# Kernel tuning notes

Measured on AMD Instinct MI355X. Metric: run time of the kernel, lower is better.

Reference implementation:

```python
import jax, jax.numpy as jnp
import numpy as np

FEATURE_SIZE = 1000000  # padding index == FEATURE_SIZE
NEG_INF = -1e9


def _attn_pool(emb_table, hist_idx, ad_idx):
    # hist_idx: [B, L] int, ad_idx: [B] int
    hist = emb_table[hist_idx]          # [B, L, K] gather
    ad = emb_table[ad_idx]              # [B, K]
    score = jnp.einsum('blk,bk->bl', hist, ad)          # [B, L]
    score = jnp.where(hist_idx != FEATURE_SIZE, score, NEG_INF)
    w = jax.nn.softmax(score, axis=1)
    return jnp.einsum('blk,bl->bk', hist, w)            # [B, K]


def setup_inputs() -> dict:
    key = jax.random.key(0)
    ks = jax.random.split(key, 12)
    B, F, K = 4096, 8, 64
    V = FEATURE_SIZE + 1
    d_in = 3 * K + F * K  # 704
    inp = {
        'feature_idx': jax.random.randint(ks[0], (B, F), 0, FEATURE_SIZE),
        'hist_item': jax.random.randint(ks[1], (B, 350), 0, V),
        'hist_author': jax.random.randint(ks[2], (B, 250), 0, V),
        'hist_music': jax.random.randint(ks[3], (B, 100), 0, V),
        'emb_table': jax.random.normal(ks[4], (V, K), jnp.float32),
        'W1': jax.random.normal(ks[5], (d_in, 512), jnp.float32) * 0.02,
        'b1': jnp.zeros((512,), jnp.float32),
        'W2': jax.random.normal(ks[6], (512, 256), jnp.float32) * 0.02,
        'b2': jnp.zeros((256,), jnp.float32),
        'W3': jax.random.normal(ks[7], (256, 128), jnp.float32) * 0.02,
        'b3': jnp.zeros((128,), jnp.float32),
        'Wo': jax.random.normal(ks[8], (128, 1), jnp.float32) * 0.02,
        'bo': jnp.zeros((1,), jnp.float32),
    }
    return inp


def reference(feature_idx, hist_item, hist_author, hist_music, emb_table,
              W1, b1, W2, b2, W3, b3, Wo, bo):
    # ad indices for the three behavior features: columns 2, 3, 6
    pools = [
        _attn_pool(emb_table, hist_item, feature_idx[:, 2]),
        _attn_pool(emb_table, hist_author, feature_idx[:, 3]),
        _attn_pool(emb_table, hist_music, feature_idx[:, 6]),
    ]
    user_beha = jnp.concatenate(pools, axis=1)                    # [B, 3K]
    B = feature_idx.shape[0]
    ad_emb = emb_table[feature_idx].reshape(B, -1)                # [B, F*K]
    x = jnp.concatenate([user_beha, ad_emb], axis=1)              # [B, 704]
    x = jax.nn.relu(x @ W1 + b1)
    x = jax.nn.relu(x @ W2 + b2)
    x = jax.nn.relu(x @ W3 + b3)
    logits = x @ Wo + bo                                          # [B, 1]
    return logits
```

## Files before the change

### kernel.cpp

```cpp
#include <hip/hip_runtime.h>
#include <cstddef>

#define BATCH   4096
#define PAD_IDX 1000000
#define NEG_INF_F (-1e9f)
#define EMB_FLOATS 64000064

typedef __attribute__((ext_vector_type(8))) short bf16x8;
typedef __attribute__((ext_vector_type(4))) float f32x4;
typedef unsigned short u16;

__device__ __forceinline__ u16 f2bf(float f) {
    unsigned u = __float_as_uint(f);
    return (u16)((u + 0x7fffu + ((u >> 16) & 1u)) >> 16);
}

#define UPD(mm, dd, aa, s, v)                          \
    {                                                  \
        float nm = fmaxf(mm, (s));                     \
        float sc = __expf(mm - nm);                    \
        float e  = __expf((s) - nm);                   \
        dd = fmaf(dd, sc, e);                          \
        aa.x = fmaf(aa.x, sc, e * (v).x);              \
        aa.y = fmaf(aa.y, sc, e * (v).y);              \
        aa.z = fmaf(aa.z, sc, e * (v).z);              \
        aa.w = fmaf(aa.w, sc, e * (v).w);              \
        mm = nm;                                       \
    }

#define MERGE(P)                                                  \
    {                                                             \
        float mo  = __shfl_xor(m, P);                             \
        float d_o = __shfl_xor(d, P);                             \
        float ax = __shfl_xor(acc.x, P);                          \
        float ay = __shfl_xor(acc.y, P);                          \
        float az = __shfl_xor(acc.z, P);                          \
        float aw = __shfl_xor(acc.w, P);                          \
        float nm = fmaxf(m, mo);                                  \
        float sA = __expf(m - nm), sB = __expf(mo - nm);          \
        d = d * sA + d_o * sB;                                    \
        acc.x = acc.x * sA + ax * sB;                             \
        acc.y = acc.y * sA + ay * sB;                             \
        acc.z = acc.z * sA + az * sB;                             \
        acc.w = acc.w * sA + aw * sB;                             \
        m = nm;                                                   \
    }

#define QRED(s)                       \
    s += __shfl_xor(s, 1);            \
    s += __shfl_xor(s, 2);            \
    s += __shfl_xor(s, 4);            \
    s += __shfl_xor(s, 8);

#define DOT4(v, a) ((v).x * (a).x + (v).y * (a).y + (v).z * (a).z + (v).w * (a).w)

__global__ void __launch_bounds__(256) prep_kernel(
    const int* __restrict__ fidx,
    const int* __restrict__ hist_item,
    const int* __restrict__ hist_author,
    const int* __restrict__ hist_music,
    const float* __restrict__ emb,
    const float* __restrict__ W1, const float* __restrict__ W2, const float* __restrict__ W3,
    u16* __restrict__ x,
    u16* __restrict__ w1t, u16* __restrict__ w2t, u16* __restrict__ w3t)
{
    __shared__ float tile[32][33];
    const int blk = blockIdx.x;
    const int tid = threadIdx.x;

    if (blk < 2048) {
        float s = 0.f;
        const size_t base = (size_t)blk * 32768 + tid * 4;
#pragma unroll 8
        for (int i = 0; i < 32; ++i) {
            const size_t fi = base + (size_t)i * 1024;
            if (fi + 4 <= EMB_FLOATS) {
                const float4 v = *(const float4*)(emb + fi);
                s += v.x + v.y + v.z + v.w;
            }
        }
        if (s == 1.2345e37f) x[0] = 1;
        return;
    }

    if (blk < 7168) {
        const int w    = (blk - 2048) * 4 + (tid >> 6);
        const int lane = tid & 63;
        const int t16  = lane & 15;
        const int q    = lane >> 4;

        if (w < 3 * BATCH) {
            const int h = w >> 12;
            const int b = w & (BATCH - 1);
            int L, col, off;
            const int* hrow;
            if (h == 0)      { L = 350; col = 2; off = 0;   hrow = hist_item   + (size_t)b * 350; }
            else if (h == 1) { L = 250; col = 3; off = 64;  hrow = hist_author + (size_t)b * 250; }
            else             { L = 100; col = 6; off = 128; hrow = hist_music  + (size_t)b * 100; }

            const int ad_idx = fidx[b * 8 + col];
            const float4 ad4 = *(const float4*)(emb + (size_t)ad_idx * 64 + 4 * t16);

            float m = NEG_INF_F, d = 0.f;
            float4 acc = make_float4(0.f, 0.f, 0.f, 0.f);
            float mB = NEG_INF_F, dB = 0.f;
            float4 aB = make_float4(0.f, 0.f, 0.f, 0.f);

            int l = 0;
            if (L >= 16) {
                int n0 = hrow[q], n1 = hrow[4 + q], n2 = hrow[8 + q], n3 = hrow[12 + q];
                while (true) {
                    const int i0 = n0, i1 = n1, i2 = n2, i3 = n3;
                    const float4 v0 = *(const float4*)(emb + (size_t)i0 * 64 + 4 * t16);
                    const float4 v1 = *(const float4*)(emb + (size_t)i1 * 64 + 4 * t16);
                    const float4 v2 = *(const float4*)(emb + (size_t)i2 * 64 + 4 * t16);
                    const float4 v3 = *(const float4*)(emb + (size_t)i3 * 64 + 4 * t16);
                    l += 16;
                    const bool more = (l + 16 <= L);
                    if (more) {
                        n0 = hrow[l + q];      n1 = hrow[l + 4 + q];
                        n2 = hrow[l + 8 + q];  n3 = hrow[l + 12 + q];
                    }
                    float s0 = DOT4(v0, ad4);
                    float s1 = DOT4(v1, ad4);
                    float s2 = DOT4(v2, ad4);
                    float s3 = DOT4(v3, ad4);
                    QRED(s0) QRED(s1) QRED(s2) QRED(s3)
                    if (i0 == PAD_IDX) s0 = NEG_INF_F;
                    if (i1 == PAD_IDX) s1 = NEG_INF_F;
                    if (i2 == PAD_IDX) s2 = NEG_INF_F;
                    if (i3 == PAD_IDX) s3 = NEG_INF_F;
                    UPD(m, d, acc, s0, v0)
                    UPD(mB, dB, aB, s1, v1)
                    UPD(m, d, acc, s2, v2)
                    UPD(mB, dB, aB, s3, v3)
                    if (!more) break;
                }
            }
            for (; l < L; l += 4) {
                const int li = l + q;
                const int i0 = (li < L) ? hrow[li] : PAD_IDX;
                const float4 v0 = *(const float4*)(emb + (size_t)i0 * 64 + 4 * t16);
                float s0 = DOT4(v0, ad4);
                QRED(s0)
                if (i0 == PAD_IDX) s0 = NEG_INF_F;
                UPD(m, d, acc, s0, v0)
            }

            {
                float nm = fmaxf(m, mB);
                float eA = __expf(m - nm), eB = __expf(mB - nm);
                d = d * eA + dB * eB;
                acc.x = acc.x * eA + aB.x * eB;
                acc.y = acc.y * eA + aB.y * eB;
                acc.z = acc.z * eA + aB.z * eB;
                acc.w = acc.w * eA + aB.w * eB;
                m = nm;
            }
            MERGE(16)
            MERGE(32)

            if (lane < 16) {
                const float inv = 1.f / d;
                uint2 p;
                p.x = (unsigned)f2bf(acc.x * inv) | ((unsigned)f2bf(acc.y * inv) << 16);
                p.y = (unsigned)f2bf(acc.z * inv) | ((unsigned)f2bf(acc.w * inv) << 16);
                *(uint2*)(x + (size_t)b * 704 + off + 4 * t16) = p;
            }
        } else {
            const int tt = w - 3 * BATCH;
            const int b  = tt >> 1;
            const int f  = ((tt & 1) << 2) + q;
            const int idx = fidx[b * 8 + f];
            const float4 v = *(const float4*)(emb + (size_t)idx * 64 + 4 * t16);
            uint2 p;
            p.x = (unsigned)f2bf(v.x) | ((unsigned)f2bf(v.y) << 16);
            p.y = (unsigned)f2bf(v.z) | ((unsigned)f2bf(v.w) << 16);
            *(uint2*)(x + (size_t)b * 704 + 192 + (size_t)f * 64 + 4 * t16) = p;
        }
        return;
    }

    int t = blk - 7168;
    const float* W; u16* WT; int K, N, tk, tn;
    if (t < 352)      { W = W1; WT = w1t; K = 704; N = 512; tk = t % 22; tn = t / 22; }
    else if (t < 480) { t -= 352; W = W2; WT = w2t; K = 512; N = 256; tk = t % 16; tn = t / 16; }
    else              { t -= 480; W = W3; WT = w3t; K = 256; N = 128; tk = t % 8;  tn = t / 8;  }
    const int k0 = tk * 32, n0 = tn * 32;
    const int tx = tid & 31, ty = tid >> 5;
#pragma unroll
    for (int j = 0; j < 4; ++j)
        tile[ty + 8 * j][tx] = W[(size_t)(k0 + ty + 8 * j) * N + n0 + tx];
    __syncthreads();
#pragma unroll
    for (int j = 0; j < 4; ++j)
        WT[(size_t)(n0 + ty + 8 * j) * K + k0 + tx] = f2bf(tile[tx][ty + 8 * j]);
}

template <int BN>
__global__ void __launch_bounds__(256) gemm_mfma(
    const u16* __restrict__ A, const u16* __restrict__ BT,
    const float* __restrict__ bias, u16* __restrict__ C,
    int M, int N, int K)
{
    constexpr int NB = BN / 16;
    __shared__ u16 As[64][40];
    __shared__ u16 Bs[BN][40];

    const int tid  = threadIdx.x;
    const int wave = tid >> 6, lane = tid & 63;
    const int quad = lane >> 4, l16 = lane & 15;
    const int bm = blockIdx.y * 64, bn = blockIdx.x * BN;

    const int srow = tid >> 2;
    const int sk   = (tid & 3) * 8;

    f32x4 acc[NB];
#pragma unroll
    for (int i = 0; i < NB; ++i) acc[i] = (f32x4){0.f, 0.f, 0.f, 0.f};

    const size_t a_base = (size_t)(bm + srow) * K + sk;

    for (int k0 = 0; k0 < K; k0 += 32) {
        *(float4*)&As[srow][sk] = *(const float4*)(A + a_base + k0);
#pragma unroll
        for (int r0 = 0; r0 < BN; r0 += 64) {
            *(float4*)&Bs[r0 + srow][sk] =
                *(const float4*)(BT + (size_t)(bn + r0 + srow) * K + k0 + sk);
        }
        __syncthreads();

        const bf16x8 af = *(const bf16x8*)&As[wave * 16 + l16][quad * 8];
#pragma unroll
        for (int ni = 0; ni < NB; ++ni) {
            const bf16x8 bf = *(const bf16x8*)&Bs[ni * 16 + l16][quad * 8];
            acc[ni] = __builtin_amdgcn_mfma_f32_16x16x32_bf16(af, bf, acc[ni], 0, 0, 0);
        }
        __syncthreads();
    }

#pragma unroll
    for (int ni = 0; ni < NB; ++ni) {
        const int col = bn + ni * 16 + l16;
        const float bv = bias[col];
#pragma unroll
        for (int r = 0; r < 4; ++r) {
            const int row = bm + wave * 16 + quad * 4 + r;
            float v = fmaxf(acc[ni][r] + bv, 0.f);
            C[(size_t)row * N + col] = f2bf(v);
        }
    }
}

__global__ void __launch_bounds__(256) tail_mlp(
    const u16* __restrict__ h1, const u16* __restrict__ W2T, const u16* __restrict__ W3T,
    const float* __restrict__ b2, const float* __restrict__ b3,
    const float* __restrict__ Wo, const float* __restrict__ bo,
    float* __restrict__ out)
{
    __shared__ u16 As16[16][40];
    __shared__ u16 Bs[256][40];
    __shared__ u16 h2s[16][264];
    __shared__ float psum[16][4];

    const int tid  = threadIdx.x;
    const int wave = tid >> 6, lane = tid & 63;
    const int quad = lane >> 4, l16 = lane & 15;
    const int r0 = blockIdx.x * 16;

    f32x4 acc2[4];
#pragma unroll
    for (int i = 0; i < 4; ++i) acc2[i] = (f32x4){0.f, 0.f, 0.f, 0.f};

    for (int k0 = 0; k0 < 512; k0 += 32) {
        if (tid < 64)
            *(float4*)&As16[tid >> 2][(tid & 3) * 8] =
                *(const float4*)(h1 + (size_t)(r0 + (tid >> 2)) * 512 + k0 + (tid & 3) * 8);
        {
            const u16* src = W2T + (size_t)tid * 512 + k0;
#pragma unroll
            for (int c = 0; c < 4; ++c)
                *(float4*)&Bs[tid][c * 8] = *(const float4*)(src + c * 8);
        }
        __syncthreads();

        const bf16x8 af = *(const bf16x8*)&As16[l16][quad * 8];
#pragma unroll
        for (int ni = 0; ni < 4; ++ni) {
            const bf16x8 bf = *(const bf16x8*)&Bs[wave * 64 + ni * 16 + l16][quad * 8];
            acc2[ni] = __builtin_amdgcn_mfma_f32_16x16x32_bf16(af, bf, acc2[ni], 0, 0, 0);
        }
        __syncthreads();
    }

#pragma unroll
    for (int ni = 0; ni < 4; ++ni) {
        const int col = wave * 64 + ni * 16 + l16;
        const float bv = b2[col];
#pragma unroll
        for (int r = 0; r < 4; ++r)
            h2s[quad * 4 + r][col] = f2bf(fmaxf(acc2[ni][r] + bv, 0.f));
    }
    __syncthreads();

    f32x4 acc3[2];
#pragma unroll
    for (int i = 0; i < 2; ++i) acc3[i] = (f32x4){0.f, 0.f, 0.f, 0.f};

    for (int k0 = 0; k0 < 256; k0 += 32) {
        if (tid < 128) {
            const u16* src = W3T + (size_t)tid * 256 + k0;
#pragma unroll
            for (int c = 0; c < 4; ++c)
                *(float4*)&Bs[tid][c * 8] = *(const float4*)(src + c * 8);
        }
        __syncthreads();

        const bf16x8 af = *(const bf16x8*)&h2s[l16][k0 + quad * 8];
#pragma unroll
        for (int ni = 0; ni < 2; ++ni) {
            const bf16x8 bf = *(const bf16x8*)&Bs[wave * 32 + ni * 16 + l16][quad * 8];
            acc3[ni] = __builtin_amdgcn_mfma_f32_16x16x32_bf16(af, bf, acc3[ni], 0, 0, 0);
        }
        __syncthreads();
    }

    float part[4] = {0.f, 0.f, 0.f, 0.f};
#pragma unroll
    for (int ni = 0; ni < 2; ++ni) {
        const int col = wave * 32 + ni * 16 + l16;
        const float bv = b3[col];
        const float wv = Wo[col];
#pragma unroll
        for (int r = 0; r < 4; ++r)
            part[r] = fmaf(fmaxf(acc3[ni][r] + bv, 0.f), wv, part[r]);
    }
#pragma unroll
    for (int r = 0; r < 4; ++r) { QRED(part[r]) }
    if (l16 == 0) {
#pragma unroll
        for (int r = 0; r < 4; ++r)
            psum[quad * 4 + r][wave] = part[r];
    }
    __syncthreads();
    if (tid < 16)
        out[r0 + tid] = psum[tid][0] + psum[tid][1] + psum[tid][2] + psum[tid][3] + bo[0];
}

extern "C" void kernel_launch(void* const* d_in, const int* in_sizes, int n_in,
                              void* d_out, int out_size, void* d_ws, size_t ws_size,
                              hipStream_t stream) {
    const int*   fidx  = (const int*)d_in[0];
    const int*   hitem = (const int*)d_in[1];
    const int*   hauth = (const int*)d_in[2];
    const int*   hmus  = (const int*)d_in[3];
    const float* emb   = (const float*)d_in[4];
    const float* W1 = (const float*)d_in[5];
    const float* b1 = (const float*)d_in[6];
    const float* W2 = (const float*)d_in[7];
    const float* b2 = (const float*)d_in[8];
    const float* W3 = (const float*)d_in[9];
    const float* b3 = (const float*)d_in[10];
    const float* Wo = (const float*)d_in[11];
    const float* bo = (const float*)d_in[12];
    float* out = (float*)d_out;

    u16* x   = (u16*)d_ws;
    u16* h1  = x   + (size_t)BATCH * 704;
    u16* w1t = h1  + (size_t)BATCH * 512;
    u16* w2t = w1t + (size_t)704 * 512;
    u16* w3t = w2t + (size_t)512 * 256;

    prep_kernel<<<7680, 256, 0, stream>>>(fidx, hitem, hauth, hmus, emb,
                                          W1, W2, W3, x, w1t, w2t, w3t);

    gemm_mfma<64><<<dim3(512 / 64, BATCH / 64), 256, 0, stream>>>(
        x, w1t, b1, h1, BATCH, 512, 704);

    tail_mlp<<<BATCH / 16, 256, 0, stream>>>(h1, w2t, w3t, b2, b3, Wo, bo, out);
}
```

Measured before the change: 503.8 us.

## Fuse first MLP layer into tail kernel and drop full embedding-table sweep

Removes the 2048 prep blocks that streamed the entire embedding table and discarded the sum. That sweep read the whole table for no use. The W1 GEMM is folded into the tail MLP kernel, so each 16-row block computes h1 into LDS and then runs layers 2 and 3 without writing h1 to global memory or paying an extra launch. The trade-off is that every block now re-reads all of W1T from cache, since the 16-row tile gives far less weight reuse than the old 64-row GEMM tile. The larger LDS footprint may also lower occupancy.

```diff
diff --git a/kernel.cpp b/kernel.cpp
--- a/kernel.cpp
+++ b/kernel.cpp
@@ -4,7 +4,6 @@
 #define BATCH   4096
 #define PAD_IDX 1000000
 #define NEG_INF_F (-1e9f)
-#define EMB_FLOATS 64000064
 
 typedef __attribute__((ext_vector_type(8))) short bf16x8;
 typedef __attribute__((ext_vector_type(4))) float f32x4;
@@ -68,23 +67,8 @@
     const int blk = blockIdx.x;
     const int tid = threadIdx.x;
 
-    if (blk < 2048) {
-        float s = 0.f;
-        const size_t base = (size_t)blk * 32768 + tid * 4;
-#pragma unroll 8
-        for (int i = 0; i < 32; ++i) {
-            const size_t fi = base + (size_t)i * 1024;
-            if (fi + 4 <= EMB_FLOATS) {
-                const float4 v = *(const float4*)(emb + fi);
-                s += v.x + v.y + v.z + v.w;
-            }
-        }
-        if (s == 1.2345e37f) x[0] = 1;
-        return;
-    }
-
-    if (blk < 7168) {
-        const int w    = (blk - 2048) * 4 + (tid >> 6);
+    if (blk < 5120) {
+        const int w    = blk * 4 + (tid >> 6);
         const int lane = tid & 63;
         const int t16  = lane & 15;
         const int q    = lane >> 4;
@@ -181,7 +165,7 @@
         return;
     }
 
-    int t = blk - 7168;
+    int t = blk - 5120;
     const float* W; u16* WT; int K, N, tk, tn;
     if (t < 352)      { W = W1; WT = w1t; K = 704; N = 512; tk = t % 22; tn = t / 22; }
     else if (t < 480) { t -= 352; W = W2; WT = w2t; K = 512; N = 256; tk = t % 16; tn = t / 16; }
@@ -197,69 +181,16 @@
         WT[(size_t)(n0 + ty + 8 * j) * K + k0 + tx] = f2bf(tile[tx][ty + 8 * j]);
 }
 
-template <int BN>
-__global__ void __launch_bounds__(256) gemm_mfma(
-    const u16* __restrict__ A, const u16* __restrict__ BT,
-    const float* __restrict__ bias, u16* __restrict__ C,
-    int M, int N, int K)
-{
-    constexpr int NB = BN / 16;
-    __shared__ u16 As[64][40];
-    __shared__ u16 Bs[BN][40];
-
-    const int tid  = threadIdx.x;
-    const int wave = tid >> 6, lane = tid & 63;
-    const int quad = lane >> 4, l16 = lane & 15;
-    const int bm = blockIdx.y * 64, bn = blockIdx.x * BN;
-
-    const int srow = tid >> 2;
-    const int sk   = (tid & 3) * 8;
-
-    f32x4 acc[NB];
-#pragma unroll
-    for (int i = 0; i < NB; ++i) acc[i] = (f32x4){0.f, 0.f, 0.f, 0.f};
-
-    const size_t a_base = (size_t)(bm + srow) * K + sk;
-
-    for (int k0 = 0; k0 < K; k0 += 32) {
-        *(float4*)&As[srow][sk] = *(const float4*)(A + a_base + k0);
-#pragma unroll
-        for (int r0 = 0; r0 < BN; r0 += 64) {
-            *(float4*)&Bs[r0 + srow][sk] =
-                *(const float4*)(BT + (size_t)(bn + r0 + srow) * K + k0 + sk);
-        }
-        __syncthreads();
-
-        const bf16x8 af = *(const bf16x8*)&As[wave * 16 + l16][quad * 8];
-#pragma unroll
-        for (int ni = 0; ni < NB; ++ni) {
-            const bf16x8 bf = *(const bf16x8*)&Bs[ni * 16 + l16][quad * 8];
-            acc[ni] = __builtin_amdgcn_mfma_f32_16x16x32_bf16(af, bf, acc[ni], 0, 0, 0);
-        }
-        __syncthreads();
-    }
-
-#pragma unroll
-    for (int ni = 0; ni < NB; ++ni) {
-        const int col = bn + ni * 16 + l16;
-        const float bv = bias[col];
-#pragma unroll
-        for (int r = 0; r < 4; ++r) {
-            const int row = bm + wave * 16 + quad * 4 + r;
-            float v = fmaxf(acc[ni][r] + bv, 0.f);
-            C[(size_t)row * N + col] = f2bf(v);
-        }
-    }
-}
-
-__global__ void __launch_bounds__(256) tail_mlp(
-    const u16* __restrict__ h1, const u16* __restrict__ W2T, const u16* __restrict__ W3T,
-    const float* __restrict__ b2, const float* __restrict__ b3,
+__global__ void __launch_bounds__(256) fused_mlp(
+    const u16* __restrict__ x,
+    const u16* __restrict__ W1T, const u16* __restrict__ W2T, const u16* __restrict__ W3T,
+    const float* __restrict__ b1, const float* __restrict__ b2, const float* __restrict__ b3,
     const float* __restrict__ Wo, const float* __restrict__ bo,
     float* __restrict__ out)
 {
     __shared__ u16 As16[16][40];
-    __shared__ u16 Bs[256][40];
+    __shared__ u16 Bs[512][40];
+    __shared__ u16 h1s[16][520];
     __shared__ u16 h2s[16][264];
     __shared__ float psum[16][4];
 
@@ -268,14 +199,46 @@
     const int quad = lane >> 4, l16 = lane & 15;
     const int r0 = blockIdx.x * 16;
 
-    f32x4 acc2[4];
-#pragma unroll
-    for (int i = 0; i < 4; ++i) acc2[i] = (f32x4){0.f, 0.f, 0.f, 0.f};
-
-    for (int k0 = 0; k0 < 512; k0 += 32) {
+    f32x4 acc1[8];
+#pragma unroll
+    for (int i = 0; i < 8; ++i) acc1[i] = (f32x4){0.f, 0.f, 0.f, 0.f};
+
+    for (int k0 = 0; k0 < 704; k0 += 32) {
         if (tid < 64)
             *(float4*)&As16[tid >> 2][(tid & 3) * 8] =
-                *(const float4*)(h1 + (size_t)(r0 + (tid >> 2)) * 512 + k0 + (tid & 3) * 8);
+                *(const float4*)(x + (size_t)(r0 + (tid >> 2)) * 704 + k0 + (tid & 3) * 8);
+#pragma unroll
+        for (int rr = 0; rr < 512; rr += 256) {
+            const u16* src = W1T + (size_t)(rr + tid) * 704 + k0;
+#pragma unroll
+            for (int c = 0; c < 4; ++c)
+                *(float4*)&Bs[rr + tid][c * 8] = *(const float4*)(src + c * 8);
+        }
+        __syncthreads();
+
+        const bf16x8 af = *(const bf16x8*)&As16[l16][quad * 8];
+#pragma unroll
+        for (int ni = 0; ni < 8; ++ni) {
+            const bf16x8 bf = *(const bf16x8*)&Bs[wave * 128 + ni * 16 + l16][quad * 8];
+            acc1[ni] = __builtin_amdgcn_mfma_f32_16x16x32_bf16(af, bf, acc1[ni], 0, 0, 0);
+        }
+        __syncthreads();
+    }
+#pragma unroll
+    for (int ni = 0; ni < 8; ++ni) {
+        const int col = wave * 128 + ni * 16 + l16;
+        const float bv = b1[col];
+#pragma unroll
+        for (int r = 0; r < 4; ++r)
+            h1s[quad * 4 + r][col] = f2bf(fmaxf(acc1[ni][r] + bv, 0.f));
+    }
+    __syncthreads();
+
+    f32x4 acc2[4];
+#pragma unroll
+    for (int i = 0; i < 4; ++i) acc2[i] = (f32x4){0.f, 0.f, 0.f, 0.f};
+
+    for (int k0 = 0; k0 < 512; k0 += 32) {
         {
             const u16* src = W2T + (size_t)tid * 512 + k0;
 #pragma unroll
@@ -284,7 +247,7 @@
         }
         __syncthreads();
 
-        const bf16x8 af = *(const bf16x8*)&As16[l16][quad * 8];
+        const bf16x8 af = *(const bf16x8*)&h1s[l16][k0 + quad * 8];
 #pragma unroll
         for (int ni = 0; ni < 4; ++ni) {
             const bf16x8 bf = *(const bf16x8*)&Bs[wave * 64 + ni * 16 + l16][quad * 8];
@@ -292,7 +255,6 @@
         }
         __syncthreads();
     }
-
 #pragma unroll
     for (int ni = 0; ni < 4; ++ni) {
         const int col = wave * 64 + ni * 16 + l16;
@@ -366,16 +328,13 @@
     float* out = (float*)d_out;
 
     u16* x   = (u16*)d_ws;
-    u16* h1  = x   + (size_t)BATCH * 704;
-    u16* w1t = h1  + (size_t)BATCH * 512;
+    u16* w1t = x   + (size_t)BATCH * 704;
     u16* w2t = w1t + (size_t)704 * 512;
     u16* w3t = w2t + (size_t)512 * 256;
 
-    prep_kernel<<<7680, 256, 0, stream>>>(fidx, hitem, hauth, hmus, emb,
+    prep_kernel<<<5632, 256, 0, stream>>>(fidx, hitem, hauth, hmus, emb,
                                           W1, W2, W3, x, w1t, w2t, w3t);
 
-    gemm_mfma<64><<<dim3(512 / 64, BATCH / 64), 256, 0, stream>>>(
-        x, w1t, b1, h1, BATCH, 512, 704);
-
-    tail_mlp<<<BATCH / 16, 256, 0, stream>>>(h1, w2t, w3t, b2, b3, Wo, bo, out);
+    fused_mlp<<<BATCH / 16, 256, 0, stream>>>(x, w1t, w2t, w3t,
+                                              b1, b2, b3, Wo, bo, out);
 }
```

After: 461.1 us. 1.09x faster.
